# Performance work log

Hardware: AMD Instinct MI355X
Metric: run time of the kernel (lower is better)

## Reference

```python
import jax, jax.numpy as jnp
import numpy as np

H = 256   # lstm2 hidden size
D_IN = 512  # lstm2 input size (256 fed-back out + 256 audio)
BN_EPS = 1e-5


def _lstm_cell(x, h, c, Wih, Whh, bih, bhh):
    # torch gate order: i, f, g, o
    z = x @ Wih.T + h @ Whh.T + bih + bhh  # (B, 4H)
    i, f, g, o = jnp.split(z, 4, axis=-1)
    i = jax.nn.sigmoid(i)
    f = jax.nn.sigmoid(f)
    g = jnp.tanh(g)
    o = jax.nn.sigmoid(o)
    c = f * c + i * g
    h = o * jnp.tanh(c)
    return h, c


def setup_inputs() -> dict:
    key = jax.random.key(0)
    ks = jax.random.split(key, 16)
    B, T, L = 256, 512, 16
    s = 0.05
    inp = {
        "rt": jax.random.normal(ks[0], (B, H), jnp.float32),
        "audio": jax.random.normal(ks[1], (B, T, H), jnp.float32),
        "s_rt": jax.random.normal(ks[2], (B, L, H), jnp.float32),
        # lstm2 layer 0
        "W_ih_l0": jax.random.normal(ks[3], (4 * H, D_IN), jnp.float32) * s,
        "W_hh_l0": jax.random.normal(ks[4], (4 * H, H), jnp.float32) * s,
        "b_ih_l0": jax.random.normal(ks[5], (4 * H,), jnp.float32) * s,
        "b_hh_l0": jax.random.normal(ks[6], (4 * H,), jnp.float32) * s,
        # lstm2 layer 1
        "W_ih_l1": jax.random.normal(ks[7], (4 * H, H), jnp.float32) * s,
        "W_hh_l1": jax.random.normal(ks[8], (4 * H, H), jnp.float32) * s,
        "b_ih_l1": jax.random.normal(ks[9], (4 * H,), jnp.float32) * s,
        "b_hh_l1": jax.random.normal(ks[10], (4 * H,), jnp.float32) * s,
        # rt_linear head: Linear(256,128) -> BN(128) -> ReLU -> Linear(128,6)
        "W1": jax.random.normal(ks[11], (128, H), jnp.float32) * s,
        "b1": jax.random.normal(ks[12], (128,), jnp.float32) * s,
        "gamma": jnp.ones((128,), jnp.float32),
        "beta": jnp.zeros((128,), jnp.float32),
        "W2": jax.random.normal(ks[13], (6, 128), jnp.float32) * s,
        "b2": jax.random.normal(ks[14], (6,), jnp.float32) * s,
        "max_len": 0,
    }
    return inp


def reference(rt, audio, s_rt,
              W_ih_l0, W_hh_l0, b_ih_l0, b_hh_l0,
              W_ih_l1, W_hh_l1, b_ih_l1, b_hh_l1,
              W1, b1, gamma, beta, W2, b2, max_len):
    B, T, _ = audio.shape
    prev_out = jnp.mean(s_rt, axis=1)  # (B, 256): torch.mean(s_rt, dim=1)
    h1 = c1 = h2 = c2 = jnp.zeros((B, H), audio.dtype)

    def step(carry, a_t):
        prev_out, h1, c1, h2, c2 = carry
        x = jnp.concatenate([prev_out, a_t], axis=-1)  # (B, 512)
        h1n, c1n = _lstm_cell(x, h1, c1, W_ih_l0, W_hh_l0, b_ih_l0, b_hh_l0)
        h2n, c2n = _lstm_cell(h1n, h2, c2, W_ih_l1, W_hh_l1, b_ih_l1, b_hh_l1)
        return (h2n, h1n, c1n, h2n, c2n), h2n

    audio_tm = jnp.transpose(audio, (1, 0, 2))  # (T, B, 256) time-major
    _, out_tm = jax.lax.scan(step, (prev_out, h1, c1, h2, c2), audio_tm)
    out = jnp.transpose(out_tm, (1, 0, 2)).reshape(-1, H)  # (B*T, 256)

    # rt_linear head, BatchNorm1d in training mode (batch stats)
    y = out @ W1.T + b1  # (B*T, 128)
    mu = jnp.mean(y, axis=0)
    var = jnp.var(y, axis=0)
    y = (y - mu) * jax.lax.rsqrt(var + BN_EPS) * gamma + beta
    y = jax.nn.relu(y)
    y = y @ W2.T + b2  # (B*T, 6)
    return y.reshape(B, T, -1)
```

## Files before the change

### kernel.cpp

```cpp
#include <hip/hip_runtime.h>
#include <stdint.h>

typedef unsigned int u32;
typedef unsigned long long u64;
typedef _Float16 f16;
typedef _Float16 h2_t __attribute__((ext_vector_type(2)));
typedef _Float16 f16x4 __attribute__((ext_vector_type(4)));
typedef _Float16 f16x8 __attribute__((ext_vector_type(8)));
typedef float f32x4 __attribute__((ext_vector_type(4)));
typedef float f32x16 __attribute__((ext_vector_type(16)));

#define TT 512
#define NF 128
#define NTOT (256 * TT)

#define OFF_WA0   0u
#define OFF_WA1   1572864u
#define OFF_WAH   2621440u
#define OFF_GSUM  2883584u
#define OFF_GSQ   2884096u
#define OFF_CTR   2884608u
#define OFF_GH1   2886656u
#define OFF_GH2   3017728u
#define OFF_Y     3148800u

__device__ __forceinline__ float sigf(float x) { return 1.0f / (1.0f + __expf(-x)); }
__device__ __forceinline__ float tanh_fast(float x) { return 1.0f - 2.0f / (__expf(2.0f * x) + 1.0f); }

__global__ void prep_kernel(const float* __restrict__ Wih0, const float* __restrict__ Whh0,
                            const float* __restrict__ Wih1, const float* __restrict__ Whh1,
                            const float* __restrict__ W1,
                            f16* __restrict__ WA0, f16* __restrict__ WA1, f16* __restrict__ WAH,
                            float* __restrict__ gz, u32* __restrict__ ctr) {
    int idx = blockIdx.x * 256 + threadIdx.x;
    const int n0 = 786432, n1 = 524288, n2 = 131072;
    if (idx < n0) {
        int u = idx >> 9, r9 = idx & 511;
        int lane = r9 >> 3, j = r9 & 7;
        int ks = u % 6; u /= 6;
        int kw = u & 7, w = u >> 3;
        int lr = lane & 31, h = lane >> 5;
        int r = ((lr >> 3) << 8) + 8 * w + (lr & 7);
        int c = 96 * kw + 16 * ks + 8 * h + j;
        float v = (c < 512) ? Wih0[r * 512 + c] : Whh0[r * 256 + (c - 512)];
        WA0[idx] = (f16)v;
    } else if (idx < n0 + n1) {
        int i2 = idx - n0;
        int u = i2 >> 9, r9 = i2 & 511;
        int lane = r9 >> 3, j = r9 & 7;
        int ks = u & 3; u >>= 2;
        int kw = u & 7, w = u >> 3;
        int lr = lane & 31, h = lane >> 5;
        int r = ((lr >> 3) << 8) + 8 * w + (lr & 7);
        int k = 64 * kw + 16 * ks + 8 * h + j;
        float v = (k < 256) ? Wih1[r * 256 + k] : Whh1[r * 256 + (k - 256)];
        WA1[i2] = (f16)v;
    } else if (idx < n0 + n1 + n2) {
        int i2 = idx - n0 - n1;
        int u = i2 >> 9, r9 = i2 & 511;
        int lane = r9 >> 3, j = r9 & 7;
        int ks = u & 7, w = u >> 3;
        int m = lane & 15, hh = lane >> 4;
        int k = 32 * ks + 8 * hh + j;
        float v = (m < 4) ? W1[(4 * w + m) * 256 + k] : 0.f;
        WAH[i2] = (f16)v;
    } else if (idx < n0 + n1 + n2 + 256) {
        gz[idx - n0 - n1 - n2] = 0.f;
    } else if (idx < n0 + n1 + n2 + 256 + 512) {
        ctr[idx - n0 - n1 - n2 - 256] = 0u;
    }
}

#define MFMA32(A, BP, C) (C) = __builtin_amdgcn_mfma_f32_32x32x16_f16( \
    __builtin_bit_cast(f16x8, (A)), __builtin_bit_cast(f16x8, *(const uint4*)(BP)), (C), 0, 0, 0)

#define ZZWR(KW, C) do { \
    f32x4 v0_ = {(C)[0], (C)[1], (C)[2], (C)[3]};    *(f32x4*)&zz[KW][n32][4 * h32] = v0_; \
    f32x4 v1_ = {(C)[4], (C)[5], (C)[6], (C)[7]};    *(f32x4*)&zz[KW][n32][8 + 4 * h32] = v1_; \
    f32x4 v2_ = {(C)[8], (C)[9], (C)[10], (C)[11]};  *(f32x4*)&zz[KW][n32][16 + 4 * h32] = v2_; \
    f32x4 v3_ = {(C)[12], (C)[13], (C)[14], (C)[15]}; *(f32x4*)&zz[KW][n32][24 + 4 * h32] = v3_; } while (0)

__global__ __launch_bounds__(512) void lstm_group_kernel(
    const float* __restrict__ audio, const float* __restrict__ s_rt,
    const uint4* __restrict__ WA0, const uint4* __restrict__ WA1, const uint4* __restrict__ WAH,
    const float* __restrict__ bih0, const float* __restrict__ bhh0,
    const float* __restrict__ bih1, const float* __restrict__ bhh1,
    const float* __restrict__ b1,
    f16* __restrict__ gh1, f16* __restrict__ gh2, u32* __restrict__ ctr,
    f16* __restrict__ ybuf, float* __restrict__ gsum, float* __restrict__ gsq)
{
    __shared__ f16 X[32][776];
    __shared__ float zz[8][32][36];
    __shared__ f16 hst[32][8];
    __shared__ float bc0s[32], bc1s[32], b1s[4];

    const int tid = threadIdx.x;
    const int w = blockIdx.x >> 3;
    const int g = blockIdx.x & 7;
    const int wv = tid >> 6;
    const int lane = tid & 63;
    const int n32 = lane & 31;
    const int h32 = (lane >> 5) & 1;
    const int cb = tid >> 3, cj = tid & 7;

    uint4 a0[6], a1[4], ah[8] = {};
    #pragma unroll
    for (int ks = 0; ks < 6; ++ks) a0[ks] = WA0[((w * 8 + wv) * 6 + ks) * 64 + lane];
    #pragma unroll
    for (int ks = 0; ks < 4; ++ks) a1[ks] = WA1[((w * 8 + wv) * 4 + ks) * 64 + lane];
    if (wv == 0) {
        #pragma unroll
        for (int ks = 0; ks < 8; ++ks) ah[ks] = WAH[(w * 8 + ks) * 64 + lane];
    }

    if (tid < 32) {
        int r = ((tid >> 3) << 8) + 8 * w + (tid & 7);
        bc0s[tid] = bih0[r] + bhh0[r];
        bc1s[tid] = bih1[r] + bhh1[r];
    }
    if (tid < 4) b1s[tid] = b1[4 * w + tid];

    for (int it = tid; it < 32 * 256; it += 512) {
        int b = it >> 8, c = it & 255;
        const float* sp = s_rt + ((size_t)(32 * g + b) * 16) * 256 + c;
        float s = 0.f;
        #pragma unroll
        for (int l = 0; l < 16; ++l) s += sp[l * 256];
        X[b][c] = (f16)(s * 0.0625f);
        X[b][256 + c] = (f16)audio[((size_t)(32 * g + b) * 512) * 256 + c];
    }
    for (int it = tid; it < 32 * 128; it += 512) {
        int b = it >> 7, q = it & 127;
        ((u32*)&X[b][512])[q] = 0u;
    }
    float c1 = 0.f, c2 = 0.f;
    float ys0 = 0, ys1 = 0, ys2 = 0, ys3 = 0, yq0 = 0, yq1 = 0, yq2 = 0, yq3 = 0;
    __syncthreads();

    u32* ctr1 = ctr + (g * 2 + 0) * 32;
    u32* ctr2 = ctr + (g * 2 + 1) * 32;
    u64* gh1u = (u64*)gh1;
    u64* gh2u = (u64*)gh2;

    for (int t = 0; t < TT; ++t) {
        float4 av0, av1, av2, av3;
        if (t + 1 < TT) {
            const float4* a4 = (const float4*)audio;
            int b0 = tid >> 6, q0 = tid & 63;
            size_t base = ((size_t)(t + 1)) * 64 + q0;
            av0 = a4[(size_t)(32 * g + b0) * 32768 + base];
            av1 = a4[(size_t)(32 * g + b0 + 8) * 32768 + base];
            av2 = a4[(size_t)(32 * g + b0 + 16) * 32768 + base];
            av3 = a4[(size_t)(32 * g + b0 + 24) * 32768 + base];
        }
        {
            f32x16 C = {};
            #pragma unroll
            for (int ks = 0; ks < 6; ++ks)
                MFMA32(a0[ks], &X[n32][96 * wv + 16 * ks + 8 * h32], C);
            ZZWR(wv, C);
        }
        __syncthreads();
        if (tid < 256) {
            float z0 = bc0s[cj], z1 = bc0s[8 + cj], z2 = bc0s[16 + cj], z3 = bc0s[24 + cj];
            #pragma unroll
            for (int kw = 0; kw < 8; ++kw) {
                z0 += zz[kw][cb][cj];      z1 += zz[kw][cb][8 + cj];
                z2 += zz[kw][cb][16 + cj]; z3 += zz[kw][cb][24 + cj];
            }
            float c = sigf(z1) * c1 + sigf(z0) * tanh_fast(z2);
            c1 = c;
            hst[cb][cj] = (f16)(sigf(z3) * tanh_fast(c));
        }
        __syncthreads();
        if (tid < 64) {
            u64 v = ((const u64*)hst)[tid];
            __hip_atomic_store(gh1u + (size_t)(g * 32 + (tid >> 1)) * 64 + 2 * w + (tid & 1), v,
                               __ATOMIC_RELAXED, __HIP_MEMORY_SCOPE_AGENT);
            asm volatile("s_waitcnt vmcnt(0)" ::: "memory");
        }
        if (tid == 0)
            __hip_atomic_fetch_add(ctr1, 1u, __ATOMIC_RELAXED, __HIP_MEMORY_SCOPE_AGENT);
        if (wv >= 4) {
            f32x16 C = {};
            if (t > 0) {
                #pragma unroll
                for (int ks = 0; ks < 4; ++ks)
                    MFMA32(a1[ks], &X[n32][64 * (wv - 4) + 16 * ks + 8 * h32], C);
            }
            ZZWR(wv, C);
        }
        if (tid == 0) {
            u32 tgt = 32u * (u32)(t + 1);
            int guard_ = 0;
            while (__hip_atomic_load(ctr1, __ATOMIC_RELAXED, __HIP_MEMORY_SCOPE_AGENT) < tgt
                   && ++guard_ < 200000000) { __builtin_amdgcn_s_sleep(2); }
        }
        __syncthreads();
        {
            int b0 = tid >> 6, q0 = tid & 63;
            #pragma unroll
            for (int s = 0; s < 4; ++s) {
                int b = b0 + 8 * s;
                u64 v = __hip_atomic_load(gh1u + (size_t)(g * 32 + b) * 64 + q0,
                                          __ATOMIC_RELAXED, __HIP_MEMORY_SCOPE_AGENT);
                *(u64*)&X[b][512 + 4 * q0] = v;
            }
        }
        __syncthreads();
        if (wv < 4) {
            f32x16 C = {};
            #pragma unroll
            for (int ks = 0; ks < 4; ++ks)
                MFMA32(a1[ks], &X[n32][512 + 64 * wv + 16 * ks + 8 * h32], C);
            ZZWR(wv, C);
        }
        __syncthreads();
        if (tid < 256) {
            float z0 = bc1s[cj], z1 = bc1s[8 + cj], z2 = bc1s[16 + cj], z3 = bc1s[24 + cj];
            #pragma unroll
            for (int kw = 0; kw < 8; ++kw) {
                z0 += zz[kw][cb][cj];      z1 += zz[kw][cb][8 + cj];
                z2 += zz[kw][cb][16 + cj]; z3 += zz[kw][cb][24 + cj];
            }
            float c = sigf(z1) * c2 + sigf(z0) * tanh_fast(z2);
            c2 = c;
            hst[cb][cj] = (f16)(sigf(z3) * tanh_fast(c));
        }
        __syncthreads();
        if (tid < 64) {
            u64 v = ((const u64*)hst)[tid];
            __hip_atomic_store(gh2u + (size_t)(g * 32 + (tid >> 1)) * 64 + 2 * w + (tid & 1), v,
                               __ATOMIC_RELAXED, __HIP_MEMORY_SCOPE_AGENT);
            asm volatile("s_waitcnt vmcnt(0)" ::: "memory");
        }
        if (tid == 0) {
            __hip_atomic_fetch_add(ctr2, 1u, __ATOMIC_RELAXED, __HIP_MEMORY_SCOPE_AGENT);
            u32 tgt = 32u * (u32)(t + 1);
            int guard_ = 0;
            while (__hip_atomic_load(ctr2, __ATOMIC_RELAXED, __HIP_MEMORY_SCOPE_AGENT) < tgt
                   && ++guard_ < 200000000) { __builtin_amdgcn_s_sleep(2); }
        }
        __syncthreads();
        {
            int b0 = tid >> 6, q0 = tid & 63;
            #pragma unroll
            for (int s = 0; s < 4; ++s) {
                int b = b0 + 8 * s;
                u64 v = __hip_atomic_load(gh2u + (size_t)(g * 32 + b) * 64 + q0,
                                          __ATOMIC_RELAXED, __HIP_MEMORY_SCOPE_AGENT);
                *(u64*)&X[b][4 * q0] = v;
            }
            if (t + 1 < TT) {
                #define AST(AV, S) do { \
                    int b_ = (tid >> 6) + 8 * (S); int q_ = tid & 63; \
                    h2_t p0_; p0_.x = (f16)(AV).x; p0_.y = (f16)(AV).y; \
                    h2_t p1_; p1_.x = (f16)(AV).z; p1_.y = (f16)(AV).w; \
                    uint2 pv_; pv_.x = __builtin_bit_cast(u32, p0_); pv_.y = __builtin_bit_cast(u32, p1_); \
                    *(uint2*)&X[b_][256 + 4 * q_] = pv_; } while (0)
                AST(av0, 0); AST(av1, 1); AST(av2, 2); AST(av3, 3);
            }
        }
        __syncthreads();
        if (wv == 0) {
            #pragma unroll
            for (int nt = 0; nt < 2; ++nt) {
                f32x4 C = {};
                #pragma unroll
                for (int ks = 0; ks < 8; ++ks)
                    C = __builtin_amdgcn_mfma_f32_16x16x32_f16(
                        __builtin_bit_cast(f16x8, ah[ks]),
                        __builtin_bit_cast(f16x8,
                            *(const uint4*)&X[nt * 16 + (lane & 15)][32 * ks + 8 * ((lane >> 4) & 3)]),
                        C, 0, 0, 0);
                if (lane < 16) {
                    float y0 = C[0] + b1s[0], y1 = C[1] + b1s[1];
                    float y2 = C[2] + b1s[2], y3 = C[3] + b1s[3];
                    ys0 += y0; yq0 += y0 * y0; ys1 += y1; yq1 += y1 * y1;
                    ys2 += y2; yq2 += y2 * y2; ys3 += y3; yq3 += y3 * y3;
                    f16x4 yp; yp[0] = (f16)y0; yp[1] = (f16)y1; yp[2] = (f16)y2; yp[3] = (f16)y3;
                    int b = nt * 16 + lane;
                    ((u64*)ybuf)[((size_t)(g * 32 + b) * 512 + t) * 32 + w] = __builtin_bit_cast(u64, yp);
                }
            }
        }
    }
    if (wv == 0 && lane < 16) {
        #pragma unroll
        for (int m = 8; m >= 1; m >>= 1) {
            ys0 += __shfl_xor(ys0, m, 64); ys1 += __shfl_xor(ys1, m, 64);
            ys2 += __shfl_xor(ys2, m, 64); ys3 += __shfl_xor(ys3, m, 64);
            yq0 += __shfl_xor(yq0, m, 64); yq1 += __shfl_xor(yq1, m, 64);
            yq2 += __shfl_xor(yq2, m, 64); yq3 += __shfl_xor(yq3, m, 64);
        }
        if (lane == 0) {
            atomicAdd(&gsum[4 * w + 0], ys0); atomicAdd(&gsum[4 * w + 1], ys1);
            atomicAdd(&gsum[4 * w + 2], ys2); atomicAdd(&gsum[4 * w + 3], ys3);
            atomicAdd(&gsq[4 * w + 0], yq0); atomicAdd(&gsq[4 * w + 1], yq1);
            atomicAdd(&gsq[4 * w + 2], yq2); atomicAdd(&gsq[4 * w + 3], yq3);
        }
    }
}

__global__ __launch_bounds__(256) void head_kernel(
    const f16* __restrict__ ybuf, const float* __restrict__ gsum, const float* __restrict__ gsq,
    const float* __restrict__ gamma, const float* __restrict__ beta,
    const float* __restrict__ W2, const float* __restrict__ b2,
    float* __restrict__ out)
{
    __shared__ float sc[NF], sh[NF], W2s[6 * NF], b2s[6];
    const int tid = threadIdx.x;
    if (tid < NF) {
        const float invN = 1.f / (float)NTOT;
        float mu = gsum[tid] * invN;
        float var = gsq[tid] * invN - mu * mu;
        float iv = rsqrtf(var + 1e-5f);
        float s = gamma[tid] * iv;
        sc[tid] = s;
        sh[tid] = beta[tid] - mu * s;
    }
    for (int i = tid; i < 6 * NF; i += 256) W2s[i] = W2[i];
    if (tid < 6) b2s[tid] = b2[tid];
    __syncthreads();

    size_t n = (size_t)blockIdx.x * 256 + tid;
    const h2_t* yr = (const h2_t*)(ybuf + n * NF);
    float a0 = b2s[0], a1 = b2s[1], a2 = b2s[2], a3 = b2s[3], a4 = b2s[4], a5 = b2s[5];
    #pragma unroll 8
    for (int p = 0; p < 64; ++p) {
        h2_t v = yr[p];
        int f0 = 2 * p, f1 = 2 * p + 1;
        float v0 = fmaxf(fmaf((float)v.x, sc[f0], sh[f0]), 0.f);
        float v1 = fmaxf(fmaf((float)v.y, sc[f1], sh[f1]), 0.f);
        a0 = fmaf(v0, W2s[0 * NF + f0], a0); a0 = fmaf(v1, W2s[0 * NF + f1], a0);
        a1 = fmaf(v0, W2s[1 * NF + f0], a1); a1 = fmaf(v1, W2s[1 * NF + f1], a1);
        a2 = fmaf(v0, W2s[2 * NF + f0], a2); a2 = fmaf(v1, W2s[2 * NF + f1], a2);
        a3 = fmaf(v0, W2s[3 * NF + f0], a3); a3 = fmaf(v1, W2s[3 * NF + f1], a3);
        a4 = fmaf(v0, W2s[4 * NF + f0], a4); a4 = fmaf(v1, W2s[4 * NF + f1], a4);
        a5 = fmaf(v0, W2s[5 * NF + f0], a5); a5 = fmaf(v1, W2s[5 * NF + f1], a5);
    }
    float* op = out + n * 6;
    op[0] = a0; op[1] = a1; op[2] = a2; op[3] = a3; op[4] = a4; op[5] = a5;
}

extern "C" void kernel_launch(void* const* d_in, const int* in_sizes, int n_in,
                              void* d_out, int out_size, void* d_ws, size_t ws_size,
                              hipStream_t stream) {
    const float* audio = (const float*)d_in[1];
    const float* s_rt  = (const float*)d_in[2];
    const float* Wih0  = (const float*)d_in[3];
    const float* Whh0  = (const float*)d_in[4];
    const float* bih0  = (const float*)d_in[5];
    const float* bhh0  = (const float*)d_in[6];
    const float* Wih1  = (const float*)d_in[7];
    const float* Whh1  = (const float*)d_in[8];
    const float* bih1  = (const float*)d_in[9];
    const float* bhh1  = (const float*)d_in[10];
    const float* W1    = (const float*)d_in[11];
    const float* b1    = (const float*)d_in[12];
    const float* gamma = (const float*)d_in[13];
    const float* beta  = (const float*)d_in[14];
    const float* W2    = (const float*)d_in[15];
    const float* b2    = (const float*)d_in[16];

    char* ws = (char*)d_ws;
    f16* WA0    = (f16*)(ws + OFF_WA0);
    f16* WA1    = (f16*)(ws + OFF_WA1);
    f16* WAH    = (f16*)(ws + OFF_WAH);
    float* gsum = (float*)(ws + OFF_GSUM);
    float* gsq  = (float*)(ws + OFF_GSQ);
    u32* ctrp   = (u32*)(ws + OFF_CTR);
    f16* gh1    = (f16*)(ws + OFF_GH1);
    f16* gh2    = (f16*)(ws + OFF_GH2);
    f16* ybuf   = (f16*)(ws + OFF_Y);
    float* out  = (float*)d_out;

    prep_kernel<<<5635, 256, 0, stream>>>(Wih0, Whh0, Wih1, Whh1, W1,
                                          WA0, WA1, WAH, gsum, ctrp);

    lstm_group_kernel<<<256, 512, 0, stream>>>(audio, s_rt,
                                               (const uint4*)WA0, (const uint4*)WA1, (const uint4*)WAH,
                                               bih0, bhh0, bih1, bhh1, b1,
                                               gh1, gh2, ctrp, ybuf, gsum, gsq);

    head_kernel<<<NTOT / 256, 256, 0, stream>>>(ybuf, gsum, gsq, gamma, beta, W2, b2, out);
}
```

Measured before the change: 3.565 ms.

## Replace counter barriers with step-tagged hidden-state words polled per thread

Cross-block synchronisation no longer uses a shared atomic counter plus a single-thread spin and block barriers. Each hidden-state f16 pair is now stored as a 64-bit word carrying the timestep tag, and every thread polls its own words until the tags match. This removes the fetch_add, the serialised spin, and the extra __syncthreads and LDS staging on each layer's exchange. The zz buffer gains separate slots so the layer-1 recurrent partial sums can be computed before the layer-0 exchange completes. In exchange, the exchange buffers double in size and every thread issues polling loads, which adds memory traffic.

```diff
diff --git a/kernel.cpp b/kernel.cpp
--- a/kernel.cpp
+++ b/kernel.cpp
@@ -2,6 +2,7 @@
 #include <stdint.h>
 
 typedef unsigned int u32;
+typedef unsigned short u16;
 typedef unsigned long long u64;
 typedef _Float16 f16;
 typedef _Float16 h2_t __attribute__((ext_vector_type(2)));
@@ -19,10 +20,9 @@
 #define OFF_WAH   2621440u
 #define OFF_GSUM  2883584u
 #define OFF_GSQ   2884096u
-#define OFF_CTR   2884608u
-#define OFF_GH1   2886656u
-#define OFF_GH2   3017728u
-#define OFF_Y     3148800u
+#define OFF_GH1   2884608u
+#define OFF_GH2   3146752u
+#define OFF_Y     3408896u
 
 __device__ __forceinline__ float sigf(float x) { return 1.0f / (1.0f + __expf(-x)); }
 __device__ __forceinline__ float tanh_fast(float x) { return 1.0f - 2.0f / (__expf(2.0f * x) + 1.0f); }
@@ -31,7 +31,7 @@
                             const float* __restrict__ Wih1, const float* __restrict__ Whh1,
                             const float* __restrict__ W1,
                             f16* __restrict__ WA0, f16* __restrict__ WA1, f16* __restrict__ WAH,
-                            float* __restrict__ gz, u32* __restrict__ ctr) {
+                            float* __restrict__ gz, u32* __restrict__ ghz) {
     int idx = blockIdx.x * 256 + threadIdx.x;
     const int n0 = 786432, n1 = 524288, n2 = 131072;
     if (idx < n0) {
@@ -66,8 +66,8 @@
         WAH[i2] = (f16)v;
     } else if (idx < n0 + n1 + n2 + 256) {
         gz[idx - n0 - n1 - n2] = 0.f;
-    } else if (idx < n0 + n1 + n2 + 256 + 512) {
-        ctr[idx - n0 - n1 - n2 - 256] = 0u;
+    } else if (idx < n0 + n1 + n2 + 256 + 131072) {
+        ghz[idx - n0 - n1 - n2 - 256] = 0u;
     }
 }
 
@@ -86,12 +86,11 @@
     const float* __restrict__ bih0, const float* __restrict__ bhh0,
     const float* __restrict__ bih1, const float* __restrict__ bhh1,
     const float* __restrict__ b1,
-    f16* __restrict__ gh1, f16* __restrict__ gh2, u32* __restrict__ ctr,
+    u64* __restrict__ gh1u, u64* __restrict__ gh2u,
     f16* __restrict__ ybuf, float* __restrict__ gsum, float* __restrict__ gsq)
 {
     __shared__ f16 X[32][776];
-    __shared__ float zz[8][32][36];
-    __shared__ f16 hst[32][8];
+    __shared__ float zz[12][32][36];
     __shared__ float bc0s[32], bc1s[32], b1s[4];
 
     const int tid = threadIdx.x;
@@ -103,6 +102,9 @@
     const int h32 = (lane >> 5) & 1;
     const int cb = tid >> 3, cj = tid & 7;
 
+    u64* const src1 = gh1u + (size_t)g * 4096;
+    u64* const src2 = gh2u + (size_t)g * 4096;
+
     uint4 a0[6], a1[4], ah[8] = {};
     #pragma unroll
     for (int ks = 0; ks < 6; ++ks) a0[ks] = WA0[((w * 8 + wv) * 6 + ks) * 64 + lane];
@@ -137,12 +139,8 @@
     float ys0 = 0, ys1 = 0, ys2 = 0, ys3 = 0, yq0 = 0, yq1 = 0, yq2 = 0, yq3 = 0;
     __syncthreads();
 
-    u32* ctr1 = ctr + (g * 2 + 0) * 32;
-    u32* ctr2 = ctr + (g * 2 + 1) * 32;
-    u64* gh1u = (u64*)gh1;
-    u64* gh2u = (u64*)gh2;
-
     for (int t = 0; t < TT; ++t) {
+        const u32 T = (u32)(t + 1);
         float4 av0, av1, av2, av3;
         if (t + 1 < TT) {
             const float4* a4 = (const float4*)audio;
@@ -170,17 +168,19 @@
             }
             float c = sigf(z1) * c1 + sigf(z0) * tanh_fast(z2);
             c1 = c;
-            hst[cb][cj] = (f16)(sigf(z3) * tanh_fast(c));
-        }
-        __syncthreads();
-        if (tid < 64) {
-            u64 v = ((const u64*)hst)[tid];
-            __hip_atomic_store(gh1u + (size_t)(g * 32 + (tid >> 1)) * 64 + 2 * w + (tid & 1), v,
-                               __ATOMIC_RELAXED, __HIP_MEMORY_SCOPE_AGENT);
-            asm volatile("s_waitcnt vmcnt(0)" ::: "memory");
-        }
-        if (tid == 0)
-            __hip_atomic_fetch_add(ctr1, 1u, __ATOMIC_RELAXED, __HIP_MEMORY_SCOPE_AGENT);
+            f16 hf = (f16)(sigf(z3) * tanh_fast(c));
+            u32 hb = (u32)__builtin_bit_cast(u16, hf);
+            u32 nb = (u32)__shfl_xor((int)hb, 1, 64);
+            if ((tid & 1) == 0) {
+                u64 word = (u64)(hb | (nb << 16)) | ((u64)T << 32);
+                __hip_atomic_store(src1 + (cb * 128 + 4 * w + (cj >> 1)), word,
+                                   __ATOMIC_RELAXED, __HIP_MEMORY_SCOPE_AGENT);
+            }
+        }
+        u64 pv[8];
+        #pragma unroll
+        for (int i = 0; i < 8; ++i)
+            pv[i] = __hip_atomic_load(src1 + tid + 512 * i, __ATOMIC_RELAXED, __HIP_MEMORY_SCOPE_AGENT);
         if (wv >= 4) {
             f32x16 C = {};
             if (t > 0) {
@@ -188,24 +188,27 @@
                 for (int ks = 0; ks < 4; ++ks)
                     MFMA32(a1[ks], &X[n32][64 * (wv - 4) + 16 * ks + 8 * h32], C);
             }
-            ZZWR(wv, C);
-        }
-        if (tid == 0) {
-            u32 tgt = 32u * (u32)(t + 1);
-            int guard_ = 0;
-            while (__hip_atomic_load(ctr1, __ATOMIC_RELAXED, __HIP_MEMORY_SCOPE_AGENT) < tgt
-                   && ++guard_ < 200000000) { __builtin_amdgcn_s_sleep(2); }
-        }
-        __syncthreads();
+            ZZWR(wv + 4, C);
+        }
         {
-            int b0 = tid >> 6, q0 = tid & 63;
-            #pragma unroll
-            for (int s = 0; s < 4; ++s) {
-                int b = b0 + 8 * s;
-                u64 v = __hip_atomic_load(gh1u + (size_t)(g * 32 + b) * 64 + q0,
-                                          __ATOMIC_RELAXED, __HIP_MEMORY_SCOPE_AGENT);
-                *(u64*)&X[b][512 + 4 * q0] = v;
-            }
+            int guard = 0;
+            while (true) {
+                u32 stale = 0;
+                #pragma unroll
+                for (int i = 0; i < 8; ++i)
+                    if ((u32)(pv[i] >> 32) != T) stale |= (1u << i);
+                if (!stale || ++guard > 4000000) break;
+                #pragma unroll
+                for (int i = 0; i < 8; ++i)
+                    if (stale & (1u << i))
+                        pv[i] = __hip_atomic_load(src1 + tid + 512 * i,
+                                                  __ATOMIC_RELAXED, __HIP_MEMORY_SCOPE_AGENT);
+            }
+        }
+        #pragma unroll
+        for (int i = 0; i < 8; ++i) {
+            int idx = tid + 512 * i;
+            *(u32*)&X[idx >> 7][512 + 2 * (idx & 127)] = (u32)pv[i];
         }
         __syncthreads();
         if (wv < 4) {
@@ -219,47 +222,54 @@
         if (tid < 256) {
             float z0 = bc1s[cj], z1 = bc1s[8 + cj], z2 = bc1s[16 + cj], z3 = bc1s[24 + cj];
             #pragma unroll
-            for (int kw = 0; kw < 8; ++kw) {
-                z0 += zz[kw][cb][cj];      z1 += zz[kw][cb][8 + cj];
-                z2 += zz[kw][cb][16 + cj]; z3 += zz[kw][cb][24 + cj];
+            for (int kw = 0; kw < 4; ++kw) {
+                z0 += zz[kw][cb][cj] + zz[8 + kw][cb][cj];
+                z1 += zz[kw][cb][8 + cj] + zz[8 + kw][cb][8 + cj];
+                z2 += zz[kw][cb][16 + cj] + zz[8 + kw][cb][16 + cj];
+                z3 += zz[kw][cb][24 + cj] + zz[8 + kw][cb][24 + cj];
             }
             float c = sigf(z1) * c2 + sigf(z0) * tanh_fast(z2);
             c2 = c;
-            hst[cb][cj] = (f16)(sigf(z3) * tanh_fast(c));
-        }
-        __syncthreads();
-        if (tid < 64) {
-            u64 v = ((const u64*)hst)[tid];
-            __hip_atomic_store(gh2u + (size_t)(g * 32 + (tid >> 1)) * 64 + 2 * w + (tid & 1), v,
-                               __ATOMIC_RELAXED, __HIP_MEMORY_SCOPE_AGENT);
-            asm volatile("s_waitcnt vmcnt(0)" ::: "memory");
-        }
-        if (tid == 0) {
-            __hip_atomic_fetch_add(ctr2, 1u, __ATOMIC_RELAXED, __HIP_MEMORY_SCOPE_AGENT);
-            u32 tgt = 32u * (u32)(t + 1);
-            int guard_ = 0;
-            while (__hip_atomic_load(ctr2, __ATOMIC_RELAXED, __HIP_MEMORY_SCOPE_AGENT) < tgt
-                   && ++guard_ < 200000000) { __builtin_amdgcn_s_sleep(2); }
-        }
-        __syncthreads();
+            f16 hf = (f16)(sigf(z3) * tanh_fast(c));
+            u32 hb = (u32)__builtin_bit_cast(u16, hf);
+            u32 nb = (u32)__shfl_xor((int)hb, 1, 64);
+            if ((tid & 1) == 0) {
+                u64 word = (u64)(hb | (nb << 16)) | ((u64)T << 32);
+                __hip_atomic_store(src2 + (cb * 128 + 4 * w + (cj >> 1)), word,
+                                   __ATOMIC_RELAXED, __HIP_MEMORY_SCOPE_AGENT);
+            }
+        }
+        #pragma unroll
+        for (int i = 0; i < 8; ++i)
+            pv[i] = __hip_atomic_load(src2 + tid + 512 * i, __ATOMIC_RELAXED, __HIP_MEMORY_SCOPE_AGENT);
+        if (t + 1 < TT) {
+            #define AST(AV, S) do { \
+                int b_ = (tid >> 6) + 8 * (S); int q_ = tid & 63; \
+                h2_t p0_; p0_.x = (f16)(AV).x; p0_.y = (f16)(AV).y; \
+                h2_t p1_; p1_.x = (f16)(AV).z; p1_.y = (f16)(AV).w; \
+                uint2 pv_; pv_.x = __builtin_bit_cast(u32, p0_); pv_.y = __builtin_bit_cast(u32, p1_); \
+                *(uint2*)&X[b_][256 + 4 * q_] = pv_; } while (0)
+            AST(av0, 0); AST(av1, 1); AST(av2, 2); AST(av3, 3);
+        }
         {
-            int b0 = tid >> 6, q0 = tid & 63;
-            #pragma unroll
-            for (int s = 0; s < 4; ++s) {
-                int b = b0 + 8 * s;
-                u64 v = __hip_atomic_load(gh2u + (size_t)(g * 32 + b) * 64 + q0,
-                                          __ATOMIC_RELAXED, __HIP_MEMORY_SCOPE_AGENT);
-                *(u64*)&X[b][4 * q0] = v;
-            }
-            if (t + 1 < TT) {
-                #define AST(AV, S) do { \
-                    int b_ = (tid >> 6) + 8 * (S); int q_ = tid & 63; \
-                    h2_t p0_; p0_.x = (f16)(AV).x; p0_.y = (f16)(AV).y; \
-                    h2_t p1_; p1_.x = (f16)(AV).z; p1_.y = (f16)(AV).w; \
-                    uint2 pv_; pv_.x = __builtin_bit_cast(u32, p0_); pv_.y = __builtin_bit_cast(u32, p1_); \
-                    *(uint2*)&X[b_][256 + 4 * q_] = pv_; } while (0)
-                AST(av0, 0); AST(av1, 1); AST(av2, 2); AST(av3, 3);
-            }
+            int guard = 0;
+            while (true) {
+                u32 stale = 0;
+                #pragma unroll
+                for (int i = 0; i < 8; ++i)
+                    if ((u32)(pv[i] >> 32) != T) stale |= (1u << i);
+                if (!stale || ++guard > 4000000) break;
+                #pragma unroll
+                for (int i = 0; i < 8; ++i)
+                    if (stale & (1u << i))
+                        pv[i] = __hip_atomic_load(src2 + tid + 512 * i,
+                                                  __ATOMIC_RELAXED, __HIP_MEMORY_SCOPE_AGENT);
+            }
+        }
+        #pragma unroll
+        for (int i = 0; i < 8; ++i) {
+            int idx = tid + 512 * i;
+            *(u32*)&X[idx >> 7][2 * (idx & 127)] = (u32)pv[i];
         }
         __syncthreads();
         if (wv == 0) {
@@ -369,19 +379,18 @@
     f16* WAH    = (f16*)(ws + OFF_WAH);
     float* gsum = (float*)(ws + OFF_GSUM);
     float* gsq  = (float*)(ws + OFF_GSQ);
-    u32* ctrp   = (u32*)(ws + OFF_CTR);
-    f16* gh1    = (f16*)(ws + OFF_GH1);
-    f16* gh2    = (f16*)(ws + OFF_GH2);
+    u64* gh1u   = (u64*)(ws + OFF_GH1);
+    u64* gh2u   = (u64*)(ws + OFF_GH2);
     f16* ybuf   = (f16*)(ws + OFF_Y);
     float* out  = (float*)d_out;
 
-    prep_kernel<<<5635, 256, 0, stream>>>(Wih0, Whh0, Wih1, Whh1, W1,
-                                          WA0, WA1, WAH, gsum, ctrp);
+    prep_kernel<<<6145, 256, 0, stream>>>(Wih0, Whh0, Wih1, Whh1, W1,
+                                          WA0, WA1, WAH, gsum, (u32*)gh1u);
 
     lstm_group_kernel<<<256, 512, 0, stream>>>(audio, s_rt,
                                                (const uint4*)WA0, (const uint4*)WA1, (const uint4*)WAH,
                                                bih0, bhh0, bih1, bhh1, b1,
-                                               gh1, gh2, ctrp, ybuf, gsum, gsq);
+                                               gh1u, gh2u, ybuf, gsum, gsq);
 
     head_kernel<<<NTOT / 256, 256, 0, stream>>>(ybuf, gsum, gsq, gamma, beta, W2, b2, out);
 }
```

Result: slower. 5.997 ms (+68.2%).

## Restructure LSTM step to load fed-back hidden states into registers and precompute audio contributions

Applied to the files above, without the earlier changes.

The weight layout is reordered so each wave owns a contiguous K-slice for the audio, feedback and hidden inputs. Fed-back h2 and h1 fragments are now loaded from global memory straight into MFMA B registers instead of being staged through shared memory, which drops several barriers per step. The audio and h1 contributions for the next step are computed ahead of the h2 barrier, taking them off the critical path. Cross-block signalling moves to wave 7, the head matmul is split across two waves, and a shared-memory pad is added, presumably to limit occupancy or placement. The cost is more complex register-carried state and changed barrier ordering, which risks subtle races.

```diff
diff --git a/kernel.cpp b/kernel.cpp
--- a/kernel.cpp
+++ b/kernel.cpp
@@ -2,6 +2,7 @@
 #include <stdint.h>
 
 typedef unsigned int u32;
+typedef unsigned short u16;
 typedef unsigned long long u64;
 typedef _Float16 f16;
 typedef _Float16 h2_t __attribute__((ext_vector_type(2)));
@@ -38,22 +39,22 @@
         int u = idx >> 9, r9 = idx & 511;
         int lane = r9 >> 3, j = r9 & 7;
         int ks = u % 6; u /= 6;
-        int kw = u & 7, w = u >> 3;
+        int wv = u & 7, w = u >> 3;
         int lr = lane & 31, h = lane >> 5;
         int r = ((lr >> 3) << 8) + 8 * w + (lr & 7);
-        int c = 96 * kw + 16 * ks + 8 * h + j;
+        int seg = ks >> 1, sig = ks & 1;
+        int c = 256 * seg + 32 * wv + 16 * sig + 8 * h + j;
         float v = (c < 512) ? Wih0[r * 512 + c] : Whh0[r * 256 + (c - 512)];
         WA0[idx] = (f16)v;
     } else if (idx < n0 + n1) {
         int i2 = idx - n0;
-        int u = i2 >> 9, r9 = i2 & 511;
-        int lane = r9 >> 3, j = r9 & 7;
-        int ks = u & 3; u >>= 2;
-        int kw = u & 7, w = u >> 3;
+        int lane = (i2 >> 3) & 63, j = i2 & 7;
+        int ks = (i2 >> 9) & 3, wv = (i2 >> 11) & 7, w = i2 >> 14;
         int lr = lane & 31, h = lane >> 5;
         int r = ((lr >> 3) << 8) + 8 * w + (lr & 7);
-        int k = 64 * kw + 16 * ks + 8 * h + j;
-        float v = (k < 256) ? Wih1[r * 256 + k] : Whh1[r * 256 + (k - 256)];
+        int sig = ks & 1;
+        int c = 32 * wv + 16 * sig + 8 * h + j;
+        float v = (ks >> 1) ? Whh1[r * 256 + c] : Wih1[r * 256 + c];
         WA1[i2] = (f16)v;
     } else if (idx < n0 + n1 + n2) {
         int i2 = idx - n0 - n1;
@@ -71,8 +72,10 @@
     }
 }
 
-#define MFMA32(A, BP, C) (C) = __builtin_amdgcn_mfma_f32_32x32x16_f16( \
+#define MFMA32L(A, BP, C) (C) = __builtin_amdgcn_mfma_f32_32x32x16_f16( \
     __builtin_bit_cast(f16x8, (A)), __builtin_bit_cast(f16x8, *(const uint4*)(BP)), (C), 0, 0, 0)
+#define MFMA32R(A, B, C) (C) = __builtin_amdgcn_mfma_f32_32x32x16_f16( \
+    __builtin_bit_cast(f16x8, (A)), __builtin_bit_cast(f16x8, (B)), (C), 0, 0, 0)
 
 #define ZZWR(KW, C) do { \
     f32x4 v0_ = {(C)[0], (C)[1], (C)[2], (C)[3]};    *(f32x4*)&zz[KW][n32][4 * h32] = v0_; \
@@ -85,14 +88,16 @@
     const uint4* __restrict__ WA0, const uint4* __restrict__ WA1, const uint4* __restrict__ WAH,
     const float* __restrict__ bih0, const float* __restrict__ bhh0,
     const float* __restrict__ bih1, const float* __restrict__ bhh1,
-    const float* __restrict__ b1,
-    f16* __restrict__ gh1, f16* __restrict__ gh2, u32* __restrict__ ctr,
+    const float* __restrict__ b1, u32* __restrict__ ctr,
+    u64* __restrict__ gh1u, u64* __restrict__ gh2u,
     f16* __restrict__ ybuf, float* __restrict__ gsum, float* __restrict__ gsq)
 {
-    __shared__ f16 X[32][776];
+    __shared__ f16 Xa[32][264];
+    __shared__ f16 Xh2[32][264];
     __shared__ float zz[8][32][36];
     __shared__ f16 hst[32][8];
     __shared__ float bc0s[32], bc1s[32], b1s[4];
+    __shared__ float pad_[2700];
 
     const int tid = threadIdx.x;
     const int w = blockIdx.x >> 3;
@@ -101,14 +106,23 @@
     const int lane = tid & 63;
     const int n32 = lane & 31;
     const int h32 = (lane >> 5) & 1;
-    const int cb = tid >> 3, cj = tid & 7;
+    const int ct = tid - 256;
+    const int cb = ct >> 3, cj = ct & 7;
+
+    if (tid == 0) { volatile float* vp = pad_; vp[0] = 0.f; }
+
+    u32* const ctr1 = ctr + (g * 2 + 0) * 32;
+    u32* const ctr2 = ctr + (g * 2 + 1) * 32;
+    u64* const src1 = gh1u + (size_t)g * 2048;
+    u64* const src2 = gh2u + (size_t)g * 2048;
+    const size_t gbase = (size_t)n32 * 64 + 8 * wv + 2 * h32;
 
     uint4 a0[6], a1[4], ah[8] = {};
     #pragma unroll
     for (int ks = 0; ks < 6; ++ks) a0[ks] = WA0[((w * 8 + wv) * 6 + ks) * 64 + lane];
     #pragma unroll
     for (int ks = 0; ks < 4; ++ks) a1[ks] = WA1[((w * 8 + wv) * 4 + ks) * 64 + lane];
-    if (wv == 0) {
+    if (wv < 2) {
         #pragma unroll
         for (int ks = 0; ks < 8; ++ks) ah[ks] = WAH[(w * 8 + ks) * 64 + lane];
     }
@@ -126,23 +140,23 @@
         float s = 0.f;
         #pragma unroll
         for (int l = 0; l < 16; ++l) s += sp[l * 256];
-        X[b][c] = (f16)(s * 0.0625f);
-        X[b][256 + c] = (f16)audio[((size_t)(32 * g + b) * 512) * 256 + c];
-    }
-    for (int it = tid; it < 32 * 128; it += 512) {
-        int b = it >> 7, q = it & 127;
-        ((u32*)&X[b][512])[q] = 0u;
-    }
+        Xh2[b][c] = (f16)(s * 0.0625f);
+        Xa[b][c] = (f16)audio[((size_t)(32 * g + b) * 512) * 256 + c];
+    }
+    __syncthreads();
+
+    uint4 f20 = *(const uint4*)&Xh2[n32][32 * wv + 8 * h32];
+    uint4 f21 = *(const uint4*)&Xh2[n32][32 * wv + 16 + 8 * h32];
+    uint4 f10 = {0, 0, 0, 0}, f11 = {0, 0, 0, 0};
+    f32x16 aAcc = {};
+    MFMA32L(a0[2], &Xa[n32][32 * wv + 8 * h32], aAcc);
+    MFMA32L(a0[3], &Xa[n32][32 * wv + 16 + 8 * h32], aAcc);
+
     float c1 = 0.f, c2 = 0.f;
     float ys0 = 0, ys1 = 0, ys2 = 0, ys3 = 0, yq0 = 0, yq1 = 0, yq2 = 0, yq3 = 0;
-    __syncthreads();
-
-    u32* ctr1 = ctr + (g * 2 + 0) * 32;
-    u32* ctr2 = ctr + (g * 2 + 1) * 32;
-    u64* gh1u = (u64*)gh1;
-    u64* gh2u = (u64*)gh2;
 
     for (int t = 0; t < TT; ++t) {
+        const u32 T = (u32)(t + 1);
         float4 av0, av1, av2, av3;
         if (t + 1 < TT) {
             const float4* a4 = (const float4*)audio;
@@ -153,15 +167,11 @@
             av2 = a4[(size_t)(32 * g + b0 + 16) * 32768 + base];
             av3 = a4[(size_t)(32 * g + b0 + 24) * 32768 + base];
         }
-        {
-            f32x16 C = {};
-            #pragma unroll
-            for (int ks = 0; ks < 6; ++ks)
-                MFMA32(a0[ks], &X[n32][96 * wv + 16 * ks + 8 * h32], C);
-            ZZWR(wv, C);
-        }
-        __syncthreads();
-        if (tid < 256) {
+        MFMA32R(a0[0], f20, aAcc);
+        MFMA32R(a0[1], f21, aAcc);
+        ZZWR(wv, aAcc);
+        __syncthreads();
+        if (tid >= 256) {
             float z0 = bc0s[cj], z1 = bc0s[8 + cj], z2 = bc0s[16 + cj], z3 = bc0s[24 + cj];
             #pragma unroll
             for (int kw = 0; kw < 8; ++kw) {
@@ -173,50 +183,38 @@
             hst[cb][cj] = (f16)(sigf(z3) * tanh_fast(c));
         }
         __syncthreads();
-        if (tid < 64) {
-            u64 v = ((const u64*)hst)[tid];
-            __hip_atomic_store(gh1u + (size_t)(g * 32 + (tid >> 1)) * 64 + 2 * w + (tid & 1), v,
+        if (wv == 7)
+            __hip_atomic_store(src1 + (size_t)(lane >> 1) * 64 + 2 * w + (lane & 1),
+                               ((const u64*)hst)[lane],
                                __ATOMIC_RELAXED, __HIP_MEMORY_SCOPE_AGENT);
+        f32x16 Dacc = {};
+        if (t > 0) {
+            MFMA32R(a1[2], f20, Dacc);
+            MFMA32R(a1[3], f21, Dacc);
+        }
+        if (wv == 7) {
             asm volatile("s_waitcnt vmcnt(0)" ::: "memory");
-        }
-        if (tid == 0)
-            __hip_atomic_fetch_add(ctr1, 1u, __ATOMIC_RELAXED, __HIP_MEMORY_SCOPE_AGENT);
-        if (wv >= 4) {
-            f32x16 C = {};
-            if (t > 0) {
-                #pragma unroll
-                for (int ks = 0; ks < 4; ++ks)
-                    MFMA32(a1[ks], &X[n32][64 * (wv - 4) + 16 * ks + 8 * h32], C);
-            }
-            ZZWR(wv, C);
-        }
-        if (tid == 0) {
-            u32 tgt = 32u * (u32)(t + 1);
-            int guard_ = 0;
-            while (__hip_atomic_load(ctr1, __ATOMIC_RELAXED, __HIP_MEMORY_SCOPE_AGENT) < tgt
-                   && ++guard_ < 200000000) { __builtin_amdgcn_s_sleep(2); }
+            if (lane == 0) {
+                __hip_atomic_fetch_add(ctr1, 1u, __ATOMIC_RELAXED, __HIP_MEMORY_SCOPE_AGENT);
+                u32 tgt = 32u * T; int gu = 0;
+                while (__hip_atomic_load(ctr1, __ATOMIC_RELAXED, __HIP_MEMORY_SCOPE_AGENT) < tgt
+                       && ++gu < 100000000) { __builtin_amdgcn_s_sleep(1); }
+            }
         }
         __syncthreads();
         {
-            int b0 = tid >> 6, q0 = tid & 63;
-            #pragma unroll
-            for (int s = 0; s < 4; ++s) {
-                int b = b0 + 8 * s;
-                u64 v = __hip_atomic_load(gh1u + (size_t)(g * 32 + b) * 64 + q0,
-                                          __ATOMIC_RELAXED, __HIP_MEMORY_SCOPE_AGENT);
-                *(u64*)&X[b][512 + 4 * q0] = v;
-            }
-        }
-        __syncthreads();
-        if (wv < 4) {
-            f32x16 C = {};
-            #pragma unroll
-            for (int ks = 0; ks < 4; ++ks)
-                MFMA32(a1[ks], &X[n32][512 + 64 * wv + 16 * ks + 8 * h32], C);
-            ZZWR(wv, C);
-        }
-        __syncthreads();
-        if (tid < 256) {
+            u64 q0 = __hip_atomic_load(src1 + gbase + 0, __ATOMIC_RELAXED, __HIP_MEMORY_SCOPE_AGENT);
+            u64 q1 = __hip_atomic_load(src1 + gbase + 1, __ATOMIC_RELAXED, __HIP_MEMORY_SCOPE_AGENT);
+            u64 q2 = __hip_atomic_load(src1 + gbase + 4, __ATOMIC_RELAXED, __HIP_MEMORY_SCOPE_AGENT);
+            u64 q3 = __hip_atomic_load(src1 + gbase + 5, __ATOMIC_RELAXED, __HIP_MEMORY_SCOPE_AGENT);
+            f10.x = (u32)q0; f10.y = (u32)(q0 >> 32); f10.z = (u32)q1; f10.w = (u32)(q1 >> 32);
+            f11.x = (u32)q2; f11.y = (u32)(q2 >> 32); f11.z = (u32)q3; f11.w = (u32)(q3 >> 32);
+        }
+        MFMA32R(a1[0], f10, Dacc);
+        MFMA32R(a1[1], f11, Dacc);
+        ZZWR(wv, Dacc);
+        __syncthreads();
+        if (tid >= 256) {
             float z0 = bc1s[cj], z1 = bc1s[8 + cj], z2 = bc1s[16 + cj], z3 = bc1s[24 + cj];
             #pragma unroll
             for (int kw = 0; kw < 8; ++kw) {
@@ -228,64 +226,69 @@
             hst[cb][cj] = (f16)(sigf(z3) * tanh_fast(c));
         }
         __syncthreads();
-        if (tid < 64) {
-            u64 v = ((const u64*)hst)[tid];
-            __hip_atomic_store(gh2u + (size_t)(g * 32 + (tid >> 1)) * 64 + 2 * w + (tid & 1), v,
+        if (wv == 7)
+            __hip_atomic_store(src2 + (size_t)(lane >> 1) * 64 + 2 * w + (lane & 1),
+                               ((const u64*)hst)[lane],
                                __ATOMIC_RELAXED, __HIP_MEMORY_SCOPE_AGENT);
+        if (t + 1 < TT) {
+            #define AST(AV, S) do { \
+                int b_ = (tid >> 6) + 8 * (S); int q_ = tid & 63; \
+                h2_t p0_; p0_.x = (f16)(AV).x; p0_.y = (f16)(AV).y; \
+                h2_t p1_; p1_.x = (f16)(AV).z; p1_.y = (f16)(AV).w; \
+                uint2 pv_; pv_.x = __builtin_bit_cast(u32, p0_); pv_.y = __builtin_bit_cast(u32, p1_); \
+                *(uint2*)&Xa[b_][4 * q_] = pv_; } while (0)
+            AST(av0, 0); AST(av1, 1); AST(av2, 2); AST(av3, 3);
+        }
+        __syncthreads();
+        aAcc = (f32x16){};
+        if (t + 1 < TT) {
+            MFMA32L(a0[2], &Xa[n32][32 * wv + 8 * h32], aAcc);
+            MFMA32L(a0[3], &Xa[n32][32 * wv + 16 + 8 * h32], aAcc);
+            MFMA32R(a0[4], f10, aAcc);
+            MFMA32R(a0[5], f11, aAcc);
+        }
+        if (wv == 7) {
             asm volatile("s_waitcnt vmcnt(0)" ::: "memory");
-        }
-        if (tid == 0) {
-            __hip_atomic_fetch_add(ctr2, 1u, __ATOMIC_RELAXED, __HIP_MEMORY_SCOPE_AGENT);
-            u32 tgt = 32u * (u32)(t + 1);
-            int guard_ = 0;
-            while (__hip_atomic_load(ctr2, __ATOMIC_RELAXED, __HIP_MEMORY_SCOPE_AGENT) < tgt
-                   && ++guard_ < 200000000) { __builtin_amdgcn_s_sleep(2); }
+            if (lane == 0) {
+                __hip_atomic_fetch_add(ctr2, 1u, __ATOMIC_RELAXED, __HIP_MEMORY_SCOPE_AGENT);
+                u32 tgt = 32u * T; int gu = 0;
+                while (__hip_atomic_load(ctr2, __ATOMIC_RELAXED, __HIP_MEMORY_SCOPE_AGENT) < tgt
+                       && ++gu < 100000000) { __builtin_amdgcn_s_sleep(1); }
+            }
         }
         __syncthreads();
         {
-            int b0 = tid >> 6, q0 = tid & 63;
+            u64 q0 = __hip_atomic_load(src2 + gbase + 0, __ATOMIC_RELAXED, __HIP_MEMORY_SCOPE_AGENT);
+            u64 q1 = __hip_atomic_load(src2 + gbase + 1, __ATOMIC_RELAXED, __HIP_MEMORY_SCOPE_AGENT);
+            u64 q2 = __hip_atomic_load(src2 + gbase + 4, __ATOMIC_RELAXED, __HIP_MEMORY_SCOPE_AGENT);
+            u64 q3 = __hip_atomic_load(src2 + gbase + 5, __ATOMIC_RELAXED, __HIP_MEMORY_SCOPE_AGENT);
+            f20.x = (u32)q0; f20.y = (u32)(q0 >> 32); f20.z = (u32)q1; f20.w = (u32)(q1 >> 32);
+            f21.x = (u32)q2; f21.y = (u32)(q2 >> 32); f21.z = (u32)q3; f21.w = (u32)(q3 >> 32);
+            *(uint4*)&Xh2[n32][32 * wv + 8 * h32] = f20;
+            *(uint4*)&Xh2[n32][32 * wv + 16 + 8 * h32] = f21;
+        }
+        __syncthreads();
+        if (wv < 2) {
+            f32x4 C = {};
             #pragma unroll
-            for (int s = 0; s < 4; ++s) {
-                int b = b0 + 8 * s;
-                u64 v = __hip_atomic_load(gh2u + (size_t)(g * 32 + b) * 64 + q0,
-                                          __ATOMIC_RELAXED, __HIP_MEMORY_SCOPE_AGENT);
-                *(u64*)&X[b][4 * q0] = v;
-            }
-            if (t + 1 < TT) {
-                #define AST(AV, S) do { \
-                    int b_ = (tid >> 6) + 8 * (S); int q_ = tid & 63; \
-                    h2_t p0_; p0_.x = (f16)(AV).x; p0_.y = (f16)(AV).y; \
-                    h2_t p1_; p1_.x = (f16)(AV).z; p1_.y = (f16)(AV).w; \
-                    uint2 pv_; pv_.x = __builtin_bit_cast(u32, p0_); pv_.y = __builtin_bit_cast(u32, p1_); \
-                    *(uint2*)&X[b_][256 + 4 * q_] = pv_; } while (0)
-                AST(av0, 0); AST(av1, 1); AST(av2, 2); AST(av3, 3);
-            }
-        }
-        __syncthreads();
-        if (wv == 0) {
-            #pragma unroll
-            for (int nt = 0; nt < 2; ++nt) {
-                f32x4 C = {};
-                #pragma unroll
-                for (int ks = 0; ks < 8; ++ks)
-                    C = __builtin_amdgcn_mfma_f32_16x16x32_f16(
-                        __builtin_bit_cast(f16x8, ah[ks]),
-                        __builtin_bit_cast(f16x8,
-                            *(const uint4*)&X[nt * 16 + (lane & 15)][32 * ks + 8 * ((lane >> 4) & 3)]),
-                        C, 0, 0, 0);
-                if (lane < 16) {
-                    float y0 = C[0] + b1s[0], y1 = C[1] + b1s[1];
-                    float y2 = C[2] + b1s[2], y3 = C[3] + b1s[3];
-                    ys0 += y0; yq0 += y0 * y0; ys1 += y1; yq1 += y1 * y1;
-                    ys2 += y2; yq2 += y2 * y2; ys3 += y3; yq3 += y3 * y3;
-                    f16x4 yp; yp[0] = (f16)y0; yp[1] = (f16)y1; yp[2] = (f16)y2; yp[3] = (f16)y3;
-                    int b = nt * 16 + lane;
-                    ((u64*)ybuf)[((size_t)(g * 32 + b) * 512 + t) * 32 + w] = __builtin_bit_cast(u64, yp);
-                }
-            }
-        }
-    }
-    if (wv == 0 && lane < 16) {
+            for (int ks = 0; ks < 8; ++ks)
+                C = __builtin_amdgcn_mfma_f32_16x16x32_f16(
+                    __builtin_bit_cast(f16x8, ah[ks]),
+                    __builtin_bit_cast(f16x8,
+                        *(const uint4*)&Xh2[wv * 16 + (lane & 15)][32 * ks + 8 * ((lane >> 4) & 3)]),
+                    C, 0, 0, 0);
+            if (lane < 16) {
+                float y0 = C[0] + b1s[0], y1 = C[1] + b1s[1];
+                float y2 = C[2] + b1s[2], y3 = C[3] + b1s[3];
+                ys0 += y0; yq0 += y0 * y0; ys1 += y1; yq1 += y1 * y1;
+                ys2 += y2; yq2 += y2 * y2; ys3 += y3; yq3 += y3 * y3;
+                f16x4 yp; yp[0] = (f16)y0; yp[1] = (f16)y1; yp[2] = (f16)y2; yp[3] = (f16)y3;
+                int b = wv * 16 + lane;
+                ((u64*)ybuf)[((size_t)(g * 32 + b) * 512 + t) * 32 + w] = __builtin_bit_cast(u64, yp);
+            }
+        }
+    }
+    if (wv < 2 && lane < 16) {
         #pragma unroll
         for (int m = 8; m >= 1; m >>= 1) {
             ys0 += __shfl_xor(ys0, m, 64); ys1 += __shfl_xor(ys1, m, 64);
@@ -370,8 +373,8 @@
     float* gsum = (float*)(ws + OFF_GSUM);
     float* gsq  = (float*)(ws + OFF_GSQ);
     u32* ctrp   = (u32*)(ws + OFF_CTR);
-    f16* gh1    = (f16*)(ws + OFF_GH1);
-    f16* gh2    = (f16*)(ws + OFF_GH2);
+    u64* gh1u   = (u64*)(ws + OFF_GH1);
+    u64* gh2u   = (u64*)(ws + OFF_GH2);
     f16* ybuf   = (f16*)(ws + OFF_Y);
     float* out  = (float*)d_out;
 
@@ -380,8 +383,8 @@
 
     lstm_group_kernel<<<256, 512, 0, stream>>>(audio, s_rt,
                                                (const uint4*)WA0, (const uint4*)WA1, (const uint4*)WAH,
-                                               bih0, bhh0, bih1, bhh1, b1,
-                                               gh1, gh2, ctrp, ybuf, gsum, gsq);
+                                               bih0, bhh0, bih1, bhh1, b1, ctrp,
+                                               gh1u, gh2u, ybuf, gsum, gsq);
 
     head_kernel<<<NTOT / 256, 256, 0, stream>>>(ybuf, gsum, gsq, gamma, beta, W2, b2, out);
 }
```

New measurement: 3.690 ms. 3.5% more time.
